# Optimization experiments

Measured on AMD Instinct MI355X. Metric: run time of the kernel, lower is better.

## Reference

```python
import jax, jax.numpy as jnp
import numpy as np

B, T = 128, 512
H = 64          # hidden_dim
E = 64          # input_embed_dim
H4 = 4 * H


def _block_mask(in_dim, out_dim):
    # DroppedLinearV2 mask: 4 diagonal blocks, shape (4*in_dim, 4*out_dim)
    m = np.zeros((4 * in_dim, 4 * out_dim), dtype=np.float32)
    for i in range(4):
        m[i * in_dim:(i + 1) * in_dim, i * out_dim:(i + 1) * out_dim] = 1.0
    return jnp.asarray(m)


def setup_inputs() -> dict:
    key = jax.random.key(0)
    ks = jax.random.split(key, 16)
    s = 0.05
    return {
        "event": jax.random.randint(ks[0], (B, T), 0, 4),
        "time_step": jax.random.uniform(ks[1], (B, T), dtype=jnp.float32),
        "mkt_state": jax.random.randint(ks[2], (B, T), 0, 3),
        # type embedding MLP: Linear(4,E), Tanh, Linear(E,E), Tanh
        "et_W1": jax.random.normal(ks[3], (E, 4), dtype=jnp.float32) * s,
        "et_b1": jnp.zeros((E,), jnp.float32),
        "et_W2": jax.random.normal(ks[4], (E, E), dtype=jnp.float32) * s,
        "et_b2": jnp.zeros((E,), jnp.float32),
        # state embedding MLP: Linear(3,E), Tanh, Linear(E,E), Tanh
        "es_W1": jax.random.normal(ks[5], (E, 3), dtype=jnp.float32) * s,
        "es_b1": jnp.zeros((E,), jnp.float32),
        "es_W2": jax.random.normal(ks[6], (E, E), dtype=jnp.float32) * s,
        "es_b2": jnp.zeros((E,), jnp.float32),
        # 7 gates: [input_g, forget_g, output_g, input_target, forget_target, z_gate, decay]
        "g_W1": jax.random.normal(ks[7], (7, H4, E + H4), dtype=jnp.float32) * s,
        "g_b1": jnp.zeros((7, H4), jnp.float32),
        "g_W2": jax.random.normal(ks[8], (7, H4, H4), dtype=jnp.float32) * s,
        "g_b2": jnp.zeros((7, H4), jnp.float32),
        # intensity layer: DroppedLinearV2(H, 1) -> weight (4, 4H)
        "i_W": jax.random.normal(ks[9], (4, H4), dtype=jnp.float32) * s,
        "i_b": jnp.zeros((4,), jnp.float32),
    }


def _forward(event, time_step, mkt_state, et_W1, et_b1, et_W2, et_b2,
             es_W1, es_b1, es_W2, es_b2, g_W1, g_b1, g_W2, g_b2, i_W, i_b):
    seq_len = event.shape[1]
    # embeddings (mkt_state=True path): x = type_embedding + state_embedding
    oh_e = jax.nn.one_hot(event, 4, dtype=jnp.float32)
    te = jnp.tanh(jnp.tanh(oh_e @ et_W1.T + et_b1) @ et_W2.T + et_b2)
    oh_s = jax.nn.one_hot(mkt_state, 3, dtype=jnp.float32)
    se = jnp.tanh(jnp.tanh(oh_s @ es_W1.T + es_b1) @ es_W2.T + es_b2)
    x = te + se                                   # [B, T, E]

    gmask = _block_mask(H, H)                     # (4H, 4H)
    g_W2m = g_W2 * gmask.T[None]                  # effective masked gate weights
    i_Wm = i_W * _block_mask(H, 1).T              # (4, 4H)

    x_seq = jnp.swapaxes(x[:, :seq_len - 1], 0, 1)   # [T-1, B, E]
    dt_seq = time_step[:, 1:].T                      # [T-1, B]

    def step(carry, inp):
        h, c, ct = carry
        x_t, dt = inp
        v = jnp.concatenate([x_t, h], axis=1)                      # [B, E+4H]
        pre = jnp.tanh(jnp.einsum('bi,kgi->bkg', v, g_W1) + g_b1)  # [B,7,4H]
        g = jnp.einsum('bkg,kog->bko', pre, g_W2m) + g_b2          # [B,7,4H]
        inpt = jax.nn.sigmoid(g[:, 0])
        forget = jax.nn.sigmoid(g[:, 1])
        outp = jax.nn.sigmoid(g[:, 2])
        in_tg = jax.nn.sigmoid(g[:, 3])
        fg_tg = jax.nn.sigmoid(g[:, 4])
        z = jnp.tanh(g[:, 5])
        decay = jax.nn.softplus(g[:, 6])
        c_i = forget * c + inpt * z
        ct_new = fg_tg * ct + in_tg * z
        c_new = ct_new + (c_i - ct_new) * jnp.exp(-decay * dt[:, None])
        h_new = outp * jnp.tanh(c_new)
        return (h_new, c_new, ct_new), (c_i, ct_new, outp, decay, h_new)

    zero = jnp.zeros((event.shape[0], H4), jnp.float32)
    _, (cells, cell_targets, outputs, decays, h_all) = jax.lax.scan(
        step, (zero, zero, zero), (x_seq, dt_seq))

    intens = jax.nn.softplus(jnp.einsum('tbg,og->tbo', h_all, i_Wm) + i_b)
    tr = lambda a: jnp.swapaxes(a, 0, 1)  # [T-1,B,.] -> [B,T-1,.]
    return (tr(intens), tr(cells), tr(cell_targets), tr(outputs), tr(decays))


def reference(event, time_step, mkt_state, et_W1, et_b1, et_W2, et_b2,
              es_W1, es_b1, es_W2, es_b2, g_W1, g_b1, g_W2, g_b2, i_W, i_b):
    return _forward(event, time_step, mkt_state, et_W1, et_b1, et_W2, et_b2,
                    es_W1, es_b1, es_W2, es_b2, g_W1, g_b1, g_W2, g_b2, i_W, i_b)
```

## Files before the change

kernel.cpp:

```cpp
#include <hip/hip_runtime.h>
#include <stdint.h>

typedef unsigned short u16;
typedef unsigned char u8;
typedef unsigned long long u64;
typedef short s16x8 __attribute__((ext_vector_type(8)));
typedef float f32x4 __attribute__((ext_vector_type(4)));
typedef float f32x2 __attribute__((ext_vector_type(2)));
typedef unsigned int u32x4 __attribute__((ext_vector_type(4)));
typedef unsigned int u32x2 __attribute__((ext_vector_type(2)));

#define NB 128
#define NT 512
#define NH 256
#define GQ 8
#define MBQ 16
#define STEPS 511

#define WS_HBUF 0
#define WS_X12  131072
#define WS_BAR  134144

#define OFF_H     0
#define OFF_PRE   8448
#define OFF_G     24576
#define OFF_XC    55040
#define OFF_B2    78336
#define OFF_IW    80128
#define OFF_X12   80384
#define OFF_IDXA  83456
#define OFF_DTA   91648
#define SMEM_BYTES 124416

__device__ __forceinline__ u16 f2bf(float f) {
  unsigned u = __float_as_uint(f);
  u += 0x7FFFu + ((u >> 16) & 1u);
  return (u16)(u >> 16);
}
__device__ __forceinline__ float sigm(float x) { return 1.0f / (1.0f + __expf(-x)); }
__device__ __forceinline__ float tanh_fast(float x) {
  float e = __expf(2.0f * x);
  return 1.0f - 2.0f / (e + 1.0f);
}
__device__ __forceinline__ float softplus_f(float x) {
  return fmaxf(x, 0.0f) + __logf(1.0f + __expf(-fabsf(x)));
}

__global__ void ct4_prep(const float* __restrict__ etW1, const float* __restrict__ etb1,
                         const float* __restrict__ etW2, const float* __restrict__ etb2,
                         const float* __restrict__ esW1, const float* __restrict__ esb1,
                         const float* __restrict__ esW2, const float* __restrict__ esb2,
                         char* __restrict__ ws) {
  __shared__ float sT[4][64];
  __shared__ float sS[3][64];
  const int i = threadIdx.x;
  #pragma unroll
  for (int e = 0; e < 4; ++e) sT[e][i] = tanhf(etW1[i * 4 + e] + etb1[i]);
  #pragma unroll
  for (int s = 0; s < 3; ++s) sS[s][i] = tanhf(esW1[i * 3 + s] + esb1[i]);
  __syncthreads();
  float te[4], se[3];
  #pragma unroll
  for (int e = 0; e < 4; ++e) {
    float a = etb2[i];
    for (int jj = 0; jj < 64; ++jj) a += sT[e][jj] * etW2[i * 64 + jj];
    te[e] = tanhf(a);
  }
  #pragma unroll
  for (int s = 0; s < 3; ++s) {
    float a = esb2[i];
    for (int jj = 0; jj < 64; ++jj) a += sS[s][jj] * esW2[i * 64 + jj];
    se[s] = tanhf(a);
  }
  float* x12 = (float*)(ws + WS_X12);
  #pragma unroll
  for (int e = 0; e < 4; ++e)
    #pragma unroll
    for (int s = 0; s < 3; ++s) x12[(e * 3 + s) * 64 + i] = te[e] + se[s];
  u32x4* hz = (u32x4*)(ws + WS_HBUF);
  u32x4 z = {0u, 0u, 0u, 0u};
  for (int p = i; p < 65536 / 16; p += 64) hz[p] = z;
  int* bars = (int*)(ws + WS_BAR);
  for (int p = i; p < 1024; p += 64) bars[p] = 0;
}

__global__ __launch_bounds__(512, 1) void ct4_main(
    const int* __restrict__ ev, const float* __restrict__ ts, const int* __restrict__ mk,
    const float* __restrict__ gW1, const float* __restrict__ gb1,
    const float* __restrict__ gW2, const float* __restrict__ gb2,
    const float* __restrict__ iW, const float* __restrict__ ibp,
    float* __restrict__ out, char* __restrict__ ws) {
  extern __shared__ char smem[];
  u16* h_lds = (u16*)(smem + OFF_H);
  float* g_lds = (float*)(smem + OFF_G);
  float* xc_lds = (float*)(smem + OFF_XC);
  float* b2_lds = (float*)(smem + OFF_B2);
  float* iw_lds = (float*)(smem + OFF_IW);
  float* x12_lds = (float*)(smem + OFF_X12);
  u8* idx_all = (u8*)(smem + OFF_IDXA);
  float* dt_all = (float*)(smem + OFF_DTA);

  const int tid = threadIdx.x;
  const int bid = blockIdx.x;
  const int grp = bid & 7;
  const int j = bid >> 3;
  const int b0 = grp * MBQ;
  const int wave = tid >> 6;
  const int q = (tid >> 4) & 3;
  const int c = tid & 15;
  const int kloc0 = 2 * j;

  u16* hbuf = (u16*)(ws + WS_HBUF);
  int* bars = (int*)(ws + WS_BAR);
  int* myflag = bars + grp * 128 + j * 32;

  for (int p = tid; p < 12 * 64; p += 512) x12_lds[p] = ((const float*)(ws + WS_X12))[p];
  for (int p = tid; p < 16 * 264 / 2; p += 512) ((unsigned*)h_lds)[p] = 0u;
  if (tid < 448) {
    int kk = tid >> 6, o = tid & 63;
    b2_lds[kk * 64 + o] = gb2[kk * 256 + j * 64 + o];
  }
  if (tid < 64) iw_lds[tid] = iW[j * 256 + j * 64 + tid];
  const float ibj = ibp[j];
  for (int p = tid; p < STEPS * 16; p += 512) {
    int t = p >> 4, b = p & 15;
    idx_all[p] = (u8)(ev[(b0 + b) * NT + t] * 3 + mk[(b0 + b) * NT + t]);
    dt_all[p] = ts[(b0 + b) * NT + t + 1];
  }
  __syncthreads();
  if (tid < 448) {
    int kk = tid >> 6, o = tid & 63;
    const float* row = gW1 + (size_t)(kk * 256 + j * 64 + o) * 320;
    float a[12];
    float bb = gb1[kk * 256 + j * 64 + o];
    #pragma unroll
    for (int m = 0; m < 12; ++m) a[m] = bb;
    for (int i = 0; i < 64; ++i) {
      float w = row[i];
      #pragma unroll
      for (int m = 0; m < 12; ++m) a[m] += x12_lds[m * 64 + i] * w;
    }
    #pragma unroll
    for (int m = 0; m < 12; ++m) xc_lds[(kk * 64 + o) * 13 + m] = a[m];
  }

  s16x8 a1[4][8];
  s16x8 a2[4][2];
  const int k = wave;
  if (wave < 7) {
    #pragma unroll
    for (int s = 0; s < 8; ++s) {
      int kt = (s < 6) ? (s + (s >= kloc0 ? 2 : 0)) : (kloc0 + (s - 6));
      #pragma unroll
      for (int mt = 0; mt < 4; ++mt) {
        const float* p = gW1 + (size_t)(k * 256 + j * 64 + 16 * mt + c) * 320 + 64 + 32 * kt + 8 * q;
        union { s16x8 v; u16 u[8]; } fr;
        #pragma unroll
        for (int i = 0; i < 8; ++i) fr.u[i] = f2bf(p[i]);
        a1[mt][s] = fr.v;
      }
    }
    #pragma unroll
    for (int mt = 0; mt < 4; ++mt)
      #pragma unroll
      for (int kt = 0; kt < 2; ++kt) {
        const float* p = gW2 + (size_t)(k * 256 + j * 64 + 16 * mt + c) * 256 + j * 64 + 32 * kt + 8 * q;
        union { s16x8 v; u16 u[8]; } fr;
        #pragma unroll
        for (int i = 0; i < 8; ++i) fr.u[i] = f2bf(p[i]);
        a2[mt][kt] = fr.v;
      }
  }

  float ccA[2] = {0.f, 0.f};
  float cctA[2] = {0.f, 0.f};
  f32x4 acc[4] = {};
  const f32x4 fzero = {};
  __syncthreads();

  const int O_CELL = NB * STEPS * 4;
  const int SZB = NB * STEPS * NH;
  const int O_CT = O_CELL + SZB;
  const int O_OUT = O_CT + SZB;
  const int O_DEC = O_OUT + SZB;

  for (int t = 0; t < STEPS; ++t) {
    if (wave < 7) {
      #pragma unroll
      for (int s = 0; s < 6; ++s) {
        int ks = s + (s >= kloc0 ? 2 : 0);
        s16x8 bf = *(const s16x8*)&h_lds[c * 264 + 32 * ks + 8 * q];
        #pragma unroll
        for (int mt = 0; mt < 4; ++mt)
          acc[mt] = __builtin_amdgcn_mfma_f32_16x16x32_bf16(a1[mt][s], bf, acc[mt], 0, 0, 0);
      }
      u16* preW = (u16*)(smem + OFF_PRE) + k * (16 * 72);
      int midx = (int)idx_all[t * 16 + c];
      #pragma unroll
      for (int mt = 0; mt < 4; ++mt) {
        int o = 16 * mt + 4 * q;
        const float* xr = &xc_lds[(k * 64 + o) * 13 + midx];
        u16 u0 = f2bf(tanh_fast(acc[mt][0] + xr[0]));
        u16 u1 = f2bf(tanh_fast(acc[mt][1] + xr[13]));
        u16 u2 = f2bf(tanh_fast(acc[mt][2] + xr[26]));
        u16 u3 = f2bf(tanh_fast(acc[mt][3] + xr[39]));
        u32x2 pk;
        pk[0] = (unsigned)u0 | ((unsigned)u1 << 16);
        pk[1] = (unsigned)u2 | ((unsigned)u3 << 16);
        *(u32x2*)&preW[c * 72 + o] = pk;
      }
      f32x4 acc2[4] = {};
      #pragma unroll
      for (int kt = 0; kt < 2; ++kt) {
        s16x8 pf = *(const s16x8*)&preW[c * 72 + 32 * kt + 8 * q];
        #pragma unroll
        for (int mt = 0; mt < 4; ++mt)
          acc2[mt] = __builtin_amdgcn_mfma_f32_16x16x32_bf16(a2[mt][kt], pf, acc2[mt], 0, 0, 0);
      }
      #pragma unroll
      for (int mt = 0; mt < 4; ++mt)
        *(f32x4*)&g_lds[(k * 16 + c) * 68 + 16 * mt + 4 * q] = acc2[mt];
    }
    __syncthreads();

    const int b = tid >> 5, o2 = (tid & 31) * 2;
    float ip = 0.f;
    float ci[2], ctn[2], opv[2], dcv[2];
    {
      float dtv = dt_all[t * 16 + b];
      float G[7][2];
      #pragma unroll
      for (int kk = 0; kk < 7; ++kk) {
        f32x2 gg = *(const f32x2*)&g_lds[(kk * 16 + b) * 68 + o2];
        G[kk][0] = gg[0] + b2_lds[kk * 64 + o2];
        G[kk][1] = gg[1] + b2_lds[kk * 64 + o2 + 1];
      }
      float hnv[2];
      #pragma unroll
      for (int e = 0; e < 2; ++e) {
        float inp = sigm(G[0][e]);
        float fg = sigm(G[1][e]);
        float op = sigm(G[2][e]);
        float itg = sigm(G[3][e]);
        float ftg = sigm(G[4][e]);
        float z = tanh_fast(G[5][e]);
        float dc = softplus_f(G[6][e]);
        float c_i = fg * ccA[e] + inp * z;
        float c_t = ftg * cctA[e] + itg * z;
        float edv = __expf(-dc * dtv);
        float c_n = c_t + (c_i - c_t) * edv;
        float h_n = op * tanh_fast(c_n);
        ccA[e] = c_n;
        cctA[e] = c_t;
        ci[e] = c_i; ctn[e] = c_t; opv[e] = op; dcv[e] = dc;
        hnv[e] = h_n;
        ip += iw_lds[o2 + e] * h_n;
      }
      unsigned hp = (unsigned)f2bf(hnv[0]) | ((unsigned)f2bf(hnv[1]) << 16);
      if (t < STEPS - 1) {
        *(unsigned*)&h_lds[b * 264 + j * 64 + o2] = hp;
        __hip_atomic_store((unsigned*)&hbuf[((size_t)(((t + 1) & 1) * GQ + grp) * MBQ + b) * 256 + j * 64 + o2],
                           hp, __ATOMIC_RELAXED, __HIP_MEMORY_SCOPE_AGENT);
      }
    }
    __syncthreads();

    if (tid == 0 && t < STEPS - 1)
      __hip_atomic_store(myflag, t + 1, __ATOMIC_RELAXED, __HIP_MEMORY_SCOPE_AGENT);

    auto C2 = [&]() {
      size_t base = ((size_t)(b0 + b) * STEPS + t) * NH + j * 64 + o2;
      f32x2 v;
      v[0] = ci[0];  v[1] = ci[1];  *(f32x2*)&out[O_CELL + base] = v;
      v[0] = ctn[0]; v[1] = ctn[1]; *(f32x2*)&out[O_CT + base] = v;
      v[0] = opv[0]; v[1] = opv[1]; *(f32x2*)&out[O_OUT + base] = v;
      v[0] = dcv[0]; v[1] = dcv[1]; *(f32x2*)&out[O_DEC + base] = v;
      #pragma unroll
      for (int d = 1; d < 32; d <<= 1) ip += __shfl_xor(ip, d, 32);
      if ((tid & 31) == 0)
        out[((size_t)(b0 + b) * STEPS + t) * 4 + j] = softplus_f(ip + ibj);
    };

    if (t < STEPS - 1) {
      if (wave < 7) {
        #pragma unroll
        for (int mt = 0; mt < 4; ++mt) acc[mt] = fzero;
        #pragma unroll
        for (int s = 6; s < 8; ++s) {
          int ks = kloc0 + (s - 6);
          s16x8 bf = *(const s16x8*)&h_lds[c * 264 + 32 * ks + 8 * q];
          #pragma unroll
          for (int mt = 0; mt < 4; ++mt)
            acc[mt] = __builtin_amdgcn_mfma_f32_16x16x32_bf16(a1[mt][s], bf, acc[mt], 0, 0, 0);
        }
        C2();
      } else {
        C2();
        const int l = tid & 63;
        const int row = l >> 2;
        const int segb = (l & 3) * 32;
        int* f0p = bars + grp * 128 + (0 + (0 >= j)) * 32;
        int* f1p = bars + grp * 128 + (1 + (1 >= j)) * 32;
        int* f2p = bars + grp * 128 + (2 + (2 >= j)) * 32;
        for (;;) {
          int f0 = __hip_atomic_load(f0p, __ATOMIC_RELAXED, __HIP_MEMORY_SCOPE_AGENT);
          int f1 = __hip_atomic_load(f1p, __ATOMIC_RELAXED, __HIP_MEMORY_SCOPE_AGENT);
          int f2 = __hip_atomic_load(f2p, __ATOMIC_RELAXED, __HIP_MEMORY_SCOPE_AGENT);
          if (f0 > t && f1 > t && f2 > t) break;
          __builtin_amdgcn_s_sleep(1);
        }
        const char* rbase = (const char*)hbuf +
            ((size_t)(((t + 1) & 1) * GQ + grp) * MBQ + row) * 512 + segb;
        u64 dv[3][4];
        #pragma unroll
        for (int rb = 0; rb < 3; ++rb) {
          int jr = rb + (rb >= j);
          const u64* src = (const u64*)(rbase + jr * 128);
          #pragma unroll
          for (int kq = 0; kq < 4; ++kq)
            dv[rb][kq] = __hip_atomic_load(src + kq, __ATOMIC_RELAXED, __HIP_MEMORY_SCOPE_AGENT);
        }
        char* lbase = (char*)h_lds + row * 528 + segb;
        #pragma unroll
        for (int rb = 0; rb < 3; ++rb) {
          int jr = rb + (rb >= j);
          #pragma unroll
          for (int kq = 0; kq < 4; ++kq)
            *(u64*)(lbase + jr * 128 + 8 * kq) = dv[rb][kq];
        }
      }
      __syncthreads();
    } else {
      C2();
    }
  }
}

extern "C" void kernel_launch(void* const* d_in, const int* in_sizes, int n_in,
                              void* d_out, int out_size, void* d_ws, size_t ws_size,
                              hipStream_t stream) {
  const int* ev = (const int*)d_in[0];
  const float* ts = (const float*)d_in[1];
  const int* mk = (const int*)d_in[2];
  const float* etW1 = (const float*)d_in[3];
  const float* etb1 = (const float*)d_in[4];
  const float* etW2 = (const float*)d_in[5];
  const float* etb2 = (const float*)d_in[6];
  const float* esW1 = (const float*)d_in[7];
  const float* esb1 = (const float*)d_in[8];
  const float* esW2 = (const float*)d_in[9];
  const float* esb2 = (const float*)d_in[10];
  const float* gW1 = (const float*)d_in[11];
  const float* gb1 = (const float*)d_in[12];
  const float* gW2 = (const float*)d_in[13];
  const float* gb2 = (const float*)d_in[14];
  const float* iW = (const float*)d_in[15];
  const float* ibv = (const float*)d_in[16];
  char* ws = (char*)d_ws;
  float* out = (float*)d_out;

  ct4_prep<<<1, 64, 0, stream>>>(etW1, etb1, etW2, etb2, esW1, esb1, esW2, esb2, ws);
  (void)hipFuncSetAttribute((const void*)ct4_main,
                            hipFuncAttributeMaxDynamicSharedMemorySize, SMEM_BYTES);
  ct4_main<<<GQ * 4, 512, SMEM_BYTES, stream>>>(ev, ts, mk, gW1, gb1, gW2, gb2, iW, ibv, out, ws);
}
```

Baseline: 2.166 ms.

## Replace flag barrier with sequence-tagged mailbox for cross-block hidden-state exchange

Each hidden-state word is now published to global memory as a 64-bit value that carries the step number next to the packed bf16 pair. The per-block flag store and its flag polling are removed, and the consumer wave polls the data slots directly until every tag matches. This cuts one global round trip of flag-then-data from each recurrent step's critical path. In exchange, the exchange buffer doubles in size, the consumer spins on 24 loads per lane, and the sleep in the spin loop is dropped.

```diff
diff --git a/kernel.cpp b/kernel.cpp
--- a/kernel.cpp
+++ b/kernel.cpp
@@ -17,9 +17,8 @@
 #define MBQ 16
 #define STEPS 511
 
-#define WS_HBUF 0
+#define WS_OBOX 0
 #define WS_X12  131072
-#define WS_BAR  134144
 
 #define OFF_H     0
 #define OFF_PRE   8448
@@ -45,6 +44,12 @@
 __device__ __forceinline__ float softplus_f(float x) {
   return fmaxf(x, 0.0f) + __logf(1.0f + __expf(-fabsf(x)));
 }
+__device__ __forceinline__ u64 ald64(const u64* p) {
+  return __hip_atomic_load(p, __ATOMIC_RELAXED, __HIP_MEMORY_SCOPE_AGENT);
+}
+__device__ __forceinline__ void ast64(u64* p, u64 v) {
+  __hip_atomic_store(p, v, __ATOMIC_RELAXED, __HIP_MEMORY_SCOPE_AGENT);
+}
 
 __global__ void ct4_prep(const float* __restrict__ etW1, const float* __restrict__ etb1,
                          const float* __restrict__ etW2, const float* __restrict__ etb2,
@@ -77,11 +82,9 @@
   for (int e = 0; e < 4; ++e)
     #pragma unroll
     for (int s = 0; s < 3; ++s) x12[(e * 3 + s) * 64 + i] = te[e] + se[s];
-  u32x4* hz = (u32x4*)(ws + WS_HBUF);
+  u32x4* hz = (u32x4*)(ws + WS_OBOX);
   u32x4 z = {0u, 0u, 0u, 0u};
-  for (int p = i; p < 65536 / 16; p += 64) hz[p] = z;
-  int* bars = (int*)(ws + WS_BAR);
-  for (int p = i; p < 1024; p += 64) bars[p] = 0;
+  for (int p = i; p < 131072 / 16; p += 64) hz[p] = z;
 }
 
 __global__ __launch_bounds__(512, 1) void ct4_main(
@@ -110,9 +113,7 @@
   const int c = tid & 15;
   const int kloc0 = 2 * j;
 
-  u16* hbuf = (u16*)(ws + WS_HBUF);
-  int* bars = (int*)(ws + WS_BAR);
-  int* myflag = bars + grp * 128 + j * 32;
+  u64* obox = (u64*)(ws + WS_OBOX);
 
   for (int p = tid; p < 12 * 64; p += 512) x12_lds[p] = ((const float*)(ws + WS_X12))[p];
   for (int p = tid; p < 16 * 264 / 2; p += 512) ((unsigned*)h_lds)[p] = 0u;
@@ -226,6 +227,7 @@
     const int b = tid >> 5, o2 = (tid & 31) * 2;
     float ip = 0.f;
     float ci[2], ctn[2], opv[2], dcv[2];
+    unsigned hp = 0;
     {
       float dtv = dt_all[t * 16 + b];
       float G[7][2];
@@ -256,17 +258,12 @@
         hnv[e] = h_n;
         ip += iw_lds[o2 + e] * h_n;
       }
-      unsigned hp = (unsigned)f2bf(hnv[0]) | ((unsigned)f2bf(hnv[1]) << 16);
       if (t < STEPS - 1) {
+        hp = (unsigned)f2bf(hnv[0]) | ((unsigned)f2bf(hnv[1]) << 16);
         *(unsigned*)&h_lds[b * 264 + j * 64 + o2] = hp;
-        __hip_atomic_store((unsigned*)&hbuf[((size_t)(((t + 1) & 1) * GQ + grp) * MBQ + b) * 256 + j * 64 + o2],
-                           hp, __ATOMIC_RELAXED, __HIP_MEMORY_SCOPE_AGENT);
       }
     }
     __syncthreads();
-
-    if (tid == 0 && t < STEPS - 1)
-      __hip_atomic_store(myflag, t + 1, __ATOMIC_RELAXED, __HIP_MEMORY_SCOPE_AGENT);
 
     auto C2 = [&]() {
       size_t base = ((size_t)(b0 + b) * STEPS + t) * NH + j * 64 + o2;
@@ -282,6 +279,8 @@
     };
 
     if (t < STEPS - 1) {
+      ast64(&obox[(size_t)((((t + 1) & 1) * GQ + grp) * 4 + j) * 512 + b * 32 + (tid & 31)],
+            ((u64)(unsigned)(t + 1) << 32) | (u64)hp);
       if (wave < 7) {
         #pragma unroll
         for (int mt = 0; mt < 4; ++mt) acc[mt] = fzero;
@@ -298,35 +297,42 @@
         C2();
         const int l = tid & 63;
         const int row = l >> 2;
-        const int segb = (l & 3) * 32;
-        int* f0p = bars + grp * 128 + (0 + (0 >= j)) * 32;
-        int* f1p = bars + grp * 128 + (1 + (1 >= j)) * 32;
-        int* f2p = bars + grp * 128 + (2 + (2 >= j)) * 32;
+        const int seg = l & 3;
+        u64* ob = obox + (size_t)(((t + 1) & 1) * GQ + grp) * 4 * 512;
+        const int jr0 = 0 + (0 >= j), jr1 = 1 + (1 >= j), jr2 = 2 + (2 >= j);
+        u64* p0 = ob + jr0 * 512 + row * 32 + seg * 8;
+        u64* p1 = ob + jr1 * 512 + row * 32 + seg * 8;
+        u64* p2 = ob + jr2 * 512 + row * 32 + seg * 8;
+        const u64 want = (u64)(unsigned)(t + 1);
+        u64 v0[8], v1[8], v2[8];
+        unsigned pend = 0xFFFFFFu;
         for (;;) {
-          int f0 = __hip_atomic_load(f0p, __ATOMIC_RELAXED, __HIP_MEMORY_SCOPE_AGENT);
-          int f1 = __hip_atomic_load(f1p, __ATOMIC_RELAXED, __HIP_MEMORY_SCOPE_AGENT);
-          int f2 = __hip_atomic_load(f2p, __ATOMIC_RELAXED, __HIP_MEMORY_SCOPE_AGENT);
-          if (f0 > t && f1 > t && f2 > t) break;
-          __builtin_amdgcn_s_sleep(1);
+          #pragma unroll
+          for (int i = 0; i < 8; ++i) {
+            if (pend & (1u << i)) v0[i] = ald64(p0 + i);
+            if (pend & (1u << (8 + i))) v1[i] = ald64(p1 + i);
+            if (pend & (1u << (16 + i))) v2[i] = ald64(p2 + i);
+          }
+          unsigned np = 0;
+          #pragma unroll
+          for (int i = 0; i < 8; ++i) {
+            if ((v0[i] >> 32) != want) np |= (1u << i);
+            if ((v1[i] >> 32) != want) np |= (1u << (8 + i));
+            if ((v2[i] >> 32) != want) np |= (1u << (16 + i));
+          }
+          pend = np;
+          if (!pend) break;
         }
-        const char* rbase = (const char*)hbuf +
-            ((size_t)(((t + 1) & 1) * GQ + grp) * MBQ + row) * 512 + segb;
-        u64 dv[3][4];
-        #pragma unroll
-        for (int rb = 0; rb < 3; ++rb) {
-          int jr = rb + (rb >= j);
-          const u64* src = (const u64*)(rbase + jr * 128);
-          #pragma unroll
-          for (int kq = 0; kq < 4; ++kq)
-            dv[rb][kq] = __hip_atomic_load(src + kq, __ATOMIC_RELAXED, __HIP_MEMORY_SCOPE_AGENT);
-        }
-        char* lbase = (char*)h_lds + row * 528 + segb;
-        #pragma unroll
-        for (int rb = 0; rb < 3; ++rb) {
-          int jr = rb + (rb >= j);
-          #pragma unroll
-          for (int kq = 0; kq < 4; ++kq)
-            *(u64*)(lbase + jr * 128 + 8 * kq) = dv[rb][kq];
+        char* lb = (char*)h_lds + row * 528;
+        #pragma unroll
+        for (int i = 0; i < 8; i += 2) {
+          u32x2 w;
+          w[0] = (unsigned)v0[i]; w[1] = (unsigned)v0[i + 1];
+          *(u32x2*)(lb + jr0 * 128 + (seg * 8 + i) * 4) = w;
+          w[0] = (unsigned)v1[i]; w[1] = (unsigned)v1[i + 1];
+          *(u32x2*)(lb + jr1 * 128 + (seg * 8 + i) * 4) = w;
+          w[0] = (unsigned)v2[i]; w[1] = (unsigned)v2[i + 1];
+          *(u32x2*)(lb + jr2 * 128 + (seg * 8 + i) * 4) = w;
         }
       }
       __syncthreads();
```

After: 4.060 ms. 1.87x slower.

## Interleave two batch groups per block to hide cross-block hidden-state exchange

Applied to the files above, without the earlier changes.

Each block now handles two batch groups (A and B) and alternates between them. While one group's gate matmuls run on waves 0-6, wave 7 pulls the other group's remote hidden-state slices from global memory, so the inter-block wait overlaps with compute. The grid shrinks from 32 to 16 blocks. The input index and dt staging moves from a per-block LDS preload to per-step global loads. The split K-loop that handled local hidden columns early is replaced by a full 8-slice MFMA loop. The cost is half as many CUs and twice the serial work per block.

```diff
diff --git a/kernel.cpp b/kernel.cpp
--- a/kernel.cpp
+++ b/kernel.cpp
@@ -21,16 +21,15 @@
 #define WS_X12  131072
 #define WS_BAR  134144
 
-#define OFF_H     0
-#define OFF_PRE   8448
-#define OFF_G     24576
-#define OFF_XC    55040
-#define OFF_B2    78336
-#define OFF_IW    80128
-#define OFF_X12   80384
-#define OFF_IDXA  83456
-#define OFF_DTA   91648
-#define SMEM_BYTES 124416
+#define OFF_HA    0
+#define OFF_HB    8448
+#define OFF_PRE   16896
+#define OFF_G     33024
+#define OFF_XC    63488
+#define OFF_B2    86784
+#define OFF_IW    88576
+#define OFF_X12   88832
+#define SMEM_BYTES 91904
 
 __device__ __forceinline__ u16 f2bf(float f) {
   unsigned u = __float_as_uint(f);
@@ -44,6 +43,12 @@
 }
 __device__ __forceinline__ float softplus_f(float x) {
   return fmaxf(x, 0.0f) + __logf(1.0f + __expf(-fabsf(x)));
+}
+__device__ __forceinline__ int ald(const int* p) {
+  return __hip_atomic_load(p, __ATOMIC_RELAXED, __HIP_MEMORY_SCOPE_AGENT);
+}
+__device__ __forceinline__ u64 ald64(const u64* p) {
+  return __hip_atomic_load(p, __ATOMIC_RELAXED, __HIP_MEMORY_SCOPE_AGENT);
 }
 
 __global__ void ct4_prep(const float* __restrict__ etW1, const float* __restrict__ etb1,
@@ -91,50 +96,54 @@
     const float* __restrict__ iW, const float* __restrict__ ibp,
     float* __restrict__ out, char* __restrict__ ws) {
   extern __shared__ char smem[];
-  u16* h_lds = (u16*)(smem + OFF_H);
+  u16* h_ldsA = (u16*)(smem + OFF_HA);
+  u16* h_ldsB = (u16*)(smem + OFF_HB);
   float* g_lds = (float*)(smem + OFF_G);
   float* xc_lds = (float*)(smem + OFF_XC);
   float* b2_lds = (float*)(smem + OFF_B2);
   float* iw_lds = (float*)(smem + OFF_IW);
   float* x12_lds = (float*)(smem + OFF_X12);
-  u8* idx_all = (u8*)(smem + OFF_IDXA);
-  float* dt_all = (float*)(smem + OFF_DTA);
 
   const int tid = threadIdx.x;
   const int bid = blockIdx.x;
-  const int grp = bid & 7;
-  const int j = bid >> 3;
-  const int b0 = grp * MBQ;
+  const int p = bid & 3;
+  const int j = bid >> 2;
+  const int gA = p, gB = p + 4;
+  const int b0A = gA * MBQ, b0B = gB * MBQ;
   const int wave = tid >> 6;
   const int q = (tid >> 4) & 3;
   const int c = tid & 15;
-  const int kloc0 = 2 * j;
+  const int bb = tid >> 5;
+  const int o2 = (tid & 31) * 2;
 
   u16* hbuf = (u16*)(ws + WS_HBUF);
   int* bars = (int*)(ws + WS_BAR);
-  int* myflag = bars + grp * 128 + j * 32;
-
-  for (int p = tid; p < 12 * 64; p += 512) x12_lds[p] = ((const float*)(ws + WS_X12))[p];
-  for (int p = tid; p < 16 * 264 / 2; p += 512) ((unsigned*)h_lds)[p] = 0u;
+  int* flagAp = bars + gA * 128 + j * 32;
+  int* flagBp = bars + gB * 128 + j * 32;
+  const int jr0 = 0 + (0 >= j), jr1 = 1 + (1 >= j), jr2 = 2 + (2 >= j);
+  int* fA0 = bars + gA * 128 + jr0 * 32;
+  int* fA1 = bars + gA * 128 + jr1 * 32;
+  int* fA2 = bars + gA * 128 + jr2 * 32;
+  int* fB0 = bars + gB * 128 + jr0 * 32;
+  int* fB1 = bars + gB * 128 + jr1 * 32;
+  int* fB2 = bars + gB * 128 + jr2 * 32;
+
+  for (int pz = tid; pz < 12 * 64; pz += 512) x12_lds[pz] = ((const float*)(ws + WS_X12))[pz];
+  for (int pz = tid; pz < 2 * 16 * 264 / 2; pz += 512) ((unsigned*)(smem + OFF_HA))[pz] = 0u;
   if (tid < 448) {
     int kk = tid >> 6, o = tid & 63;
     b2_lds[kk * 64 + o] = gb2[kk * 256 + j * 64 + o];
   }
   if (tid < 64) iw_lds[tid] = iW[j * 256 + j * 64 + tid];
   const float ibj = ibp[j];
-  for (int p = tid; p < STEPS * 16; p += 512) {
-    int t = p >> 4, b = p & 15;
-    idx_all[p] = (u8)(ev[(b0 + b) * NT + t] * 3 + mk[(b0 + b) * NT + t]);
-    dt_all[p] = ts[(b0 + b) * NT + t + 1];
-  }
   __syncthreads();
   if (tid < 448) {
     int kk = tid >> 6, o = tid & 63;
     const float* row = gW1 + (size_t)(kk * 256 + j * 64 + o) * 320;
     float a[12];
-    float bb = gb1[kk * 256 + j * 64 + o];
-    #pragma unroll
-    for (int m = 0; m < 12; ++m) a[m] = bb;
+    float bbias = gb1[kk * 256 + j * 64 + o];
+    #pragma unroll
+    for (int m = 0; m < 12; ++m) a[m] = bbias;
     for (int i = 0; i < 64; ++i) {
       float w = row[i];
       #pragma unroll
@@ -149,33 +158,29 @@
   const int k = wave;
   if (wave < 7) {
     #pragma unroll
-    for (int s = 0; s < 8; ++s) {
-      int kt = (s < 6) ? (s + (s >= kloc0 ? 2 : 0)) : (kloc0 + (s - 6));
+    for (int s = 0; s < 8; ++s)
       #pragma unroll
       for (int mt = 0; mt < 4; ++mt) {
-        const float* p = gW1 + (size_t)(k * 256 + j * 64 + 16 * mt + c) * 320 + 64 + 32 * kt + 8 * q;
+        const float* pw = gW1 + (size_t)(k * 256 + j * 64 + 16 * mt + c) * 320 + 64 + 32 * s + 8 * q;
         union { s16x8 v; u16 u[8]; } fr;
         #pragma unroll
-        for (int i = 0; i < 8; ++i) fr.u[i] = f2bf(p[i]);
+        for (int i = 0; i < 8; ++i) fr.u[i] = f2bf(pw[i]);
         a1[mt][s] = fr.v;
       }
-    }
     #pragma unroll
     for (int mt = 0; mt < 4; ++mt)
       #pragma unroll
       for (int kt = 0; kt < 2; ++kt) {
-        const float* p = gW2 + (size_t)(k * 256 + j * 64 + 16 * mt + c) * 256 + j * 64 + 32 * kt + 8 * q;
+        const float* pw = gW2 + (size_t)(k * 256 + j * 64 + 16 * mt + c) * 256 + j * 64 + 32 * kt + 8 * q;
         union { s16x8 v; u16 u[8]; } fr;
         #pragma unroll
-        for (int i = 0; i < 8; ++i) fr.u[i] = f2bf(p[i]);
+        for (int i = 0; i < 8; ++i) fr.u[i] = f2bf(pw[i]);
         a2[mt][kt] = fr.v;
       }
   }
 
-  float ccA[2] = {0.f, 0.f};
-  float cctA[2] = {0.f, 0.f};
-  f32x4 acc[4] = {};
-  const f32x4 fzero = {};
+  float ccA[2] = {0.f, 0.f}, cctA[2] = {0.f, 0.f};
+  float ccB[2] = {0.f, 0.f}, cctB[2] = {0.f, 0.f};
   __syncthreads();
 
   const int O_CELL = NB * STEPS * 4;
@@ -184,54 +189,87 @@
   const int O_OUT = O_CT + SZB;
   const int O_DEC = O_OUT + SZB;
 
+  auto TOP = [&](const u16* hl, int midx) {
+    f32x4 acc[4] = {};
+    #pragma unroll
+    for (int s = 0; s < 8; ++s) {
+      s16x8 bf = *(const s16x8*)&hl[c * 264 + 32 * s + 8 * q];
+      #pragma unroll
+      for (int mt = 0; mt < 4; ++mt)
+        acc[mt] = __builtin_amdgcn_mfma_f32_16x16x32_bf16(a1[mt][s], bf, acc[mt], 0, 0, 0);
+    }
+    u16* preW = (u16*)(smem + OFF_PRE) + k * (16 * 72);
+    #pragma unroll
+    for (int mt = 0; mt < 4; ++mt) {
+      int o = 16 * mt + 4 * q;
+      const float* xr = &xc_lds[(k * 64 + o) * 13 + midx];
+      u16 u0 = f2bf(tanh_fast(acc[mt][0] + xr[0]));
+      u16 u1 = f2bf(tanh_fast(acc[mt][1] + xr[13]));
+      u16 u2 = f2bf(tanh_fast(acc[mt][2] + xr[26]));
+      u16 u3 = f2bf(tanh_fast(acc[mt][3] + xr[39]));
+      u32x2 pk;
+      pk[0] = (unsigned)u0 | ((unsigned)u1 << 16);
+      pk[1] = (unsigned)u2 | ((unsigned)u3 << 16);
+      *(u32x2*)&preW[c * 72 + o] = pk;
+    }
+    f32x4 acc2[4] = {};
+    #pragma unroll
+    for (int kt = 0; kt < 2; ++kt) {
+      s16x8 pf = *(const s16x8*)&preW[c * 72 + 32 * kt + 8 * q];
+      #pragma unroll
+      for (int mt = 0; mt < 4; ++mt)
+        acc2[mt] = __builtin_amdgcn_mfma_f32_16x16x32_bf16(a2[mt][kt], pf, acc2[mt], 0, 0, 0);
+    }
+    #pragma unroll
+    for (int mt = 0; mt < 4; ++mt)
+      *(f32x4*)&g_lds[(k * 16 + c) * 68 + 16 * mt + 4 * q] = acc2[mt];
+  };
+
+  auto PULL = [&](int tgt, int* q0, int* q1, int* q2, int parity, int gh, u16* hl) {
+    const int l = tid & 63;
+    const int row = l >> 2;
+    const int segb = (l & 3) * 32;
+    for (;;) {
+      int f0 = ald(q0), f1 = ald(q1), f2 = ald(q2);
+      if (f0 >= tgt && f1 >= tgt && f2 >= tgt) break;
+      __builtin_amdgcn_s_sleep(1);
+    }
+    const char* rbase = (const char*)hbuf + ((size_t)(parity * GQ + gh) * MBQ + row) * 512 + segb;
+    u64 dv[3][4];
+    #pragma unroll
+    for (int rb = 0; rb < 3; ++rb) {
+      int jr = rb + (rb >= j);
+      const u64* src = (const u64*)(rbase + jr * 128);
+      #pragma unroll
+      for (int kq = 0; kq < 4; ++kq) dv[rb][kq] = ald64(src + kq);
+    }
+    char* lbase = (char*)hl + row * 528 + segb;
+    #pragma unroll
+    for (int rb = 0; rb < 3; ++rb) {
+      int jr = rb + (rb >= j);
+      #pragma unroll
+      for (int kq = 0; kq < 4; ++kq) *(u64*)(lbase + jr * 128 + 8 * kq) = dv[rb][kq];
+    }
+  };
+
   for (int t = 0; t < STEPS; ++t) {
-    if (wave < 7) {
-      #pragma unroll
-      for (int s = 0; s < 6; ++s) {
-        int ks = s + (s >= kloc0 ? 2 : 0);
-        s16x8 bf = *(const s16x8*)&h_lds[c * 264 + 32 * ks + 8 * q];
-        #pragma unroll
-        for (int mt = 0; mt < 4; ++mt)
-          acc[mt] = __builtin_amdgcn_mfma_f32_16x16x32_bf16(a1[mt][s], bf, acc[mt], 0, 0, 0);
-      }
-      u16* preW = (u16*)(smem + OFF_PRE) + k * (16 * 72);
-      int midx = (int)idx_all[t * 16 + c];
-      #pragma unroll
-      for (int mt = 0; mt < 4; ++mt) {
-        int o = 16 * mt + 4 * q;
-        const float* xr = &xc_lds[(k * 64 + o) * 13 + midx];
-        u16 u0 = f2bf(tanh_fast(acc[mt][0] + xr[0]));
-        u16 u1 = f2bf(tanh_fast(acc[mt][1] + xr[13]));
-        u16 u2 = f2bf(tanh_fast(acc[mt][2] + xr[26]));
-        u16 u3 = f2bf(tanh_fast(acc[mt][3] + xr[39]));
-        u32x2 pk;
-        pk[0] = (unsigned)u0 | ((unsigned)u1 << 16);
-        pk[1] = (unsigned)u2 | ((unsigned)u3 << 16);
-        *(u32x2*)&preW[c * 72 + o] = pk;
-      }
-      f32x4 acc2[4] = {};
-      #pragma unroll
-      for (int kt = 0; kt < 2; ++kt) {
-        s16x8 pf = *(const s16x8*)&preW[c * 72 + 32 * kt + 8 * q];
-        #pragma unroll
-        for (int mt = 0; mt < 4; ++mt)
-          acc2[mt] = __builtin_amdgcn_mfma_f32_16x16x32_bf16(a2[mt][kt], pf, acc2[mt], 0, 0, 0);
-      }
-      #pragma unroll
-      for (int mt = 0; mt < 4; ++mt)
-        *(f32x4*)&g_lds[(k * 16 + c) * 68 + 16 * mt + 4 * q] = acc2[mt];
-    }
+    const int rA = (b0A + c) * NT + t, rB = (b0B + c) * NT + t;
+    int evA = ev[rA], mkA = mk[rA];
+    int evB = ev[rB], mkB = mk[rB];
+    float dtA = ts[(b0A + bb) * NT + t + 1];
+    float dtB = ts[(b0B + bb) * NT + t + 1];
+
+    if (wave < 7) TOP(h_ldsA, evA * 3 + mkA);
+    else if (t > 0) PULL(t, fB0, fB1, fB2, t & 1, gB, h_ldsB);
     __syncthreads();
 
-    const int b = tid >> 5, o2 = (tid & 31) * 2;
-    float ip = 0.f;
-    float ci[2], ctn[2], opv[2], dcv[2];
+    float ciA[2], ctnA[2], opvA[2], dcvA[2];
+    float ipA = 0.f;
     {
-      float dtv = dt_all[t * 16 + b];
       float G[7][2];
       #pragma unroll
       for (int kk = 0; kk < 7; ++kk) {
-        f32x2 gg = *(const f32x2*)&g_lds[(kk * 16 + b) * 68 + o2];
+        f32x2 gg = *(const f32x2*)&g_lds[(kk * 16 + bb) * 68 + o2];
         G[kk][0] = gg[0] + b2_lds[kk * 64 + o2];
         G[kk][1] = gg[1] + b2_lds[kk * 64 + o2 + 1];
       }
@@ -247,91 +285,94 @@
         float dc = softplus_f(G[6][e]);
         float c_i = fg * ccA[e] + inp * z;
         float c_t = ftg * cctA[e] + itg * z;
-        float edv = __expf(-dc * dtv);
+        float edv = __expf(-dc * dtA);
         float c_n = c_t + (c_i - c_t) * edv;
         float h_n = op * tanh_fast(c_n);
-        ccA[e] = c_n;
-        cctA[e] = c_t;
-        ci[e] = c_i; ctn[e] = c_t; opv[e] = op; dcv[e] = dc;
+        ccA[e] = c_n; cctA[e] = c_t;
+        ciA[e] = c_i; ctnA[e] = c_t; opvA[e] = op; dcvA[e] = dc;
         hnv[e] = h_n;
-        ip += iw_lds[o2 + e] * h_n;
-      }
-      unsigned hp = (unsigned)f2bf(hnv[0]) | ((unsigned)f2bf(hnv[1]) << 16);
+        ipA += iw_lds[o2 + e] * h_n;
+      }
       if (t < STEPS - 1) {
-        *(unsigned*)&h_lds[b * 264 + j * 64 + o2] = hp;
-        __hip_atomic_store((unsigned*)&hbuf[((size_t)(((t + 1) & 1) * GQ + grp) * MBQ + b) * 256 + j * 64 + o2],
-                           hp, __ATOMIC_RELAXED, __HIP_MEMORY_SCOPE_AGENT);
+        unsigned hp = (unsigned)f2bf(hnv[0]) | ((unsigned)f2bf(hnv[1]) << 16);
+        *(unsigned*)&h_ldsA[bb * 264 + j * 64 + o2] = hp;
+        __hip_atomic_store(
+            (unsigned*)&hbuf[((size_t)((((t + 1) & 1)) * GQ + gA) * MBQ + bb) * 256 + j * 64 + o2],
+            hp, __ATOMIC_RELAXED, __HIP_MEMORY_SCOPE_AGENT);
       }
     }
     __syncthreads();
-
     if (tid == 0 && t < STEPS - 1)
-      __hip_atomic_store(myflag, t + 1, __ATOMIC_RELAXED, __HIP_MEMORY_SCOPE_AGENT);
-
-    auto C2 = [&]() {
-      size_t base = ((size_t)(b0 + b) * STEPS + t) * NH + j * 64 + o2;
+      __hip_atomic_store(flagAp, t + 1, __ATOMIC_RELAXED, __HIP_MEMORY_SCOPE_AGENT);
+    {
+      size_t base = ((size_t)(b0A + bb) * STEPS + t) * NH + j * 64 + o2;
       f32x2 v;
-      v[0] = ci[0];  v[1] = ci[1];  *(f32x2*)&out[O_CELL + base] = v;
-      v[0] = ctn[0]; v[1] = ctn[1]; *(f32x2*)&out[O_CT + base] = v;
-      v[0] = opv[0]; v[1] = opv[1]; *(f32x2*)&out[O_OUT + base] = v;
-      v[0] = dcv[0]; v[1] = dcv[1]; *(f32x2*)&out[O_DEC + base] = v;
-      #pragma unroll
-      for (int d = 1; d < 32; d <<= 1) ip += __shfl_xor(ip, d, 32);
+      v[0] = ciA[0];  v[1] = ciA[1];  *(f32x2*)&out[O_CELL + base] = v;
+      v[0] = ctnA[0]; v[1] = ctnA[1]; *(f32x2*)&out[O_CT + base] = v;
+      v[0] = opvA[0]; v[1] = opvA[1]; *(f32x2*)&out[O_OUT + base] = v;
+      v[0] = dcvA[0]; v[1] = dcvA[1]; *(f32x2*)&out[O_DEC + base] = v;
+      #pragma unroll
+      for (int d = 1; d < 32; d <<= 1) ipA += __shfl_xor(ipA, d, 32);
       if ((tid & 31) == 0)
-        out[((size_t)(b0 + b) * STEPS + t) * 4 + j] = softplus_f(ip + ibj);
-    };
-
-    if (t < STEPS - 1) {
-      if (wave < 7) {
-        #pragma unroll
-        for (int mt = 0; mt < 4; ++mt) acc[mt] = fzero;
-        #pragma unroll
-        for (int s = 6; s < 8; ++s) {
-          int ks = kloc0 + (s - 6);
-          s16x8 bf = *(const s16x8*)&h_lds[c * 264 + 32 * ks + 8 * q];
-          #pragma unroll
-          for (int mt = 0; mt < 4; ++mt)
-            acc[mt] = __builtin_amdgcn_mfma_f32_16x16x32_bf16(a1[mt][s], bf, acc[mt], 0, 0, 0);
-        }
-        C2();
-      } else {
-        C2();
-        const int l = tid & 63;
-        const int row = l >> 2;
-        const int segb = (l & 3) * 32;
-        int* f0p = bars + grp * 128 + (0 + (0 >= j)) * 32;
-        int* f1p = bars + grp * 128 + (1 + (1 >= j)) * 32;
-        int* f2p = bars + grp * 128 + (2 + (2 >= j)) * 32;
-        for (;;) {
-          int f0 = __hip_atomic_load(f0p, __ATOMIC_RELAXED, __HIP_MEMORY_SCOPE_AGENT);
-          int f1 = __hip_atomic_load(f1p, __ATOMIC_RELAXED, __HIP_MEMORY_SCOPE_AGENT);
-          int f2 = __hip_atomic_load(f2p, __ATOMIC_RELAXED, __HIP_MEMORY_SCOPE_AGENT);
-          if (f0 > t && f1 > t && f2 > t) break;
-          __builtin_amdgcn_s_sleep(1);
-        }
-        const char* rbase = (const char*)hbuf +
-            ((size_t)(((t + 1) & 1) * GQ + grp) * MBQ + row) * 512 + segb;
-        u64 dv[3][4];
-        #pragma unroll
-        for (int rb = 0; rb < 3; ++rb) {
-          int jr = rb + (rb >= j);
-          const u64* src = (const u64*)(rbase + jr * 128);
-          #pragma unroll
-          for (int kq = 0; kq < 4; ++kq)
-            dv[rb][kq] = __hip_atomic_load(src + kq, __ATOMIC_RELAXED, __HIP_MEMORY_SCOPE_AGENT);
-        }
-        char* lbase = (char*)h_lds + row * 528 + segb;
-        #pragma unroll
-        for (int rb = 0; rb < 3; ++rb) {
-          int jr = rb + (rb >= j);
-          #pragma unroll
-          for (int kq = 0; kq < 4; ++kq)
-            *(u64*)(lbase + jr * 128 + 8 * kq) = dv[rb][kq];
-        }
-      }
-      __syncthreads();
-    } else {
-      C2();
+        out[((size_t)(b0A + bb) * STEPS + t) * 4 + j] = softplus_f(ipA + ibj);
+    }
+
+    if (wave < 7) TOP(h_ldsB, evB * 3 + mkB);
+    else if (t < STEPS - 1) PULL(t + 1, fA0, fA1, fA2, (t + 1) & 1, gA, h_ldsA);
+    __syncthreads();
+
+    float ciB[2], ctnB[2], opvB[2], dcvB[2];
+    float ipB = 0.f;
+    {
+      float G[7][2];
+      #pragma unroll
+      for (int kk = 0; kk < 7; ++kk) {
+        f32x2 gg = *(const f32x2*)&g_lds[(kk * 16 + bb) * 68 + o2];
+        G[kk][0] = gg[0] + b2_lds[kk * 64 + o2];
+        G[kk][1] = gg[1] + b2_lds[kk * 64 + o2 + 1];
+      }
+      float hnv[2];
+      #pragma unroll
+      for (int e = 0; e < 2; ++e) {
+        float inp = sigm(G[0][e]);
+        float fg = sigm(G[1][e]);
+        float op = sigm(G[2][e]);
+        float itg = sigm(G[3][e]);
+        float ftg = sigm(G[4][e]);
+        float z = tanh_fast(G[5][e]);
+        float dc = softplus_f(G[6][e]);
+        float c_i = fg * ccB[e] + inp * z;
+        float c_t = ftg * cctB[e] + itg * z;
+        float edv = __expf(-dc * dtB);
+        float c_n = c_t + (c_i - c_t) * edv;
+        float h_n = op * tanh_fast(c_n);
+        ccB[e] = c_n; cctB[e] = c_t;
+        ciB[e] = c_i; ctnB[e] = c_t; opvB[e] = op; dcvB[e] = dc;
+        hnv[e] = h_n;
+        ipB += iw_lds[o2 + e] * h_n;
+      }
+      if (t < STEPS - 1) {
+        unsigned hp = (unsigned)f2bf(hnv[0]) | ((unsigned)f2bf(hnv[1]) << 16);
+        *(unsigned*)&h_ldsB[bb * 264 + j * 64 + o2] = hp;
+        __hip_atomic_store(
+            (unsigned*)&hbuf[((size_t)((((t + 1) & 1)) * GQ + gB) * MBQ + bb) * 256 + j * 64 + o2],
+            hp, __ATOMIC_RELAXED, __HIP_MEMORY_SCOPE_AGENT);
+      }
+    }
+    __syncthreads();
+    if (tid == 0 && t < STEPS - 1)
+      __hip_atomic_store(flagBp, t + 1, __ATOMIC_RELAXED, __HIP_MEMORY_SCOPE_AGENT);
+    {
+      size_t base = ((size_t)(b0B + bb) * STEPS + t) * NH + j * 64 + o2;
+      f32x2 v;
+      v[0] = ciB[0];  v[1] = ciB[1];  *(f32x2*)&out[O_CELL + base] = v;
+      v[0] = ctnB[0]; v[1] = ctnB[1]; *(f32x2*)&out[O_CT + base] = v;
+      v[0] = opvB[0]; v[1] = opvB[1]; *(f32x2*)&out[O_OUT + base] = v;
+      v[0] = dcvB[0]; v[1] = dcvB[1]; *(f32x2*)&out[O_DEC + base] = v;
+      #pragma unroll
+      for (int d = 1; d < 32; d <<= 1) ipB += __shfl_xor(ipB, d, 32);
+      if ((tid & 31) == 0)
+        out[((size_t)(b0B + bb) * STEPS + t) * 4 + j] = softplus_f(ipB + ibj);
     }
   }
 }
@@ -362,5 +403,5 @@
   ct4_prep<<<1, 64, 0, stream>>>(etW1, etb1, etW2, etb2, esW1, esb1, esW2, esb2, ws);
   (void)hipFuncSetAttribute((const void*)ct4_main,
                             hipFuncAttributeMaxDynamicSharedMemorySize, SMEM_BYTES);
-  ct4_main<<<GQ * 4, 512, SMEM_BYTES, stream>>>(ev, ts, mk, gW1, gb1, gW2, gb2, iW, ibv, out, ws);
-}
+  ct4_main<<<16, 512, SMEM_BYTES, stream>>>(ev, ts, mk, gW1, gb1, gW2, gb2, iW, ibv, out, ws);
+}
```

Result: slower. 3.912 ms (+80.6%).
